# Performance work log

Measured on AMD Instinct MI355X. Metric: run time of the kernel, lower is better.

Reference implementation:

```python
import jax, jax.numpy as jnp
import numpy as np
from jax import lax

EDGE_THRESHOLD = 0.1
DILATION_SIZE = 5
VAR_RATIO_THRESHOLD = 2.0
LOCAL_WINDOW = 7

SOBEL_X = jnp.array([[-1., 0., 1.], [-2., 0., 2.], [-1., 0., 1.]], dtype=jnp.float32)[None, None]
SOBEL_Y = jnp.array([[-1., -2., -1.], [0., 0., 0.], [1., 2., 1.]], dtype=jnp.float32)[None, None]


def _conv_same(x, k):
    # x: (B,1,H,W), k: (1,1,kh,kw), stride 1, SAME padding (odd kernels)
    return lax.conv_general_dilated(x, k.astype(x.dtype), (1, 1), 'SAME',
                                    dimension_numbers=('NCHW', 'OIHW', 'NCHW'))


def _rgb_to_luminance(x):
    w = jnp.array([0.299, 0.587, 0.114], dtype=x.dtype).reshape(1, 3, 1, 1)
    return (x * w).sum(axis=1, keepdims=True)


def _sobel_edge(lum):
    gx = _conv_same(lum, SOBEL_X)
    gy = _conv_same(lum, SOBEL_Y)
    return jnp.sqrt(gx * gx + gy * gy + 1e-12)


def _local_variance(x, mask):
    ws = LOCAL_WINDOW
    ones_k = jnp.ones((1, 1, ws, ws), dtype=x.dtype)
    local_sum = _conv_same(x * mask, ones_k)
    local_cnt = jnp.clip(_conv_same(mask, ones_k), 1.0, None)
    local_mean = local_sum / local_cnt
    local_sq_sum = _conv_same(x * x * mask, ones_k)
    local_var = jnp.clip(local_sq_sum / local_cnt - local_mean ** 2, 0.0, None) * mask
    total = jnp.clip(mask.sum(axis=(2, 3)), 1.0, None)  # (B,1)
    return local_var.sum(axis=(2, 3)) / total  # (B,1)


def _compute_ringing_mask(img):
    lum = _rgb_to_luminance(img) if img.shape[1] == 3 else img
    grad_mag = _sobel_edge(lum)
    E = (grad_mag > EDGE_THRESHOLD).astype(lum.dtype)
    # morphological dilation via max pool, kernel=5, stride=1, SAME padding
    E_dilated = lax.reduce_window(E, -jnp.inf, lax.max,
                                  (1, 1, DILATION_SIZE, DILATION_SIZE),
                                  (1, 1, 1, 1), 'SAME')
    M_prox = jnp.clip(E_dilated - E, 0.0, None)
    M_bg = 1.0 - E_dilated
    var_prox = _local_variance(lum, M_prox)  # (B,1)
    var_bg = _local_variance(lum, M_bg)      # (B,1)
    ratio = var_prox / (var_bg + 1e-12)
    is_ringing = (ratio > VAR_RATIO_THRESHOLD).astype(lum.dtype)  # (B,1)
    return M_prox * is_ringing[:, :, None, None]


def setup_inputs() -> dict:
    key = jax.random.key(0)
    k1, k2 = jax.random.split(key)
    B, C, H, W = 16, 3, 512, 512
    ref = jax.random.uniform(k1, (B, C, H, W), dtype=jnp.float32)
    tgt = jax.random.uniform(k2, (B, C, H, W), dtype=jnp.float32)
    return {"ref": ref, "tgt": tgt}


def reference(ref, tgt):
    ringing_ref = _compute_ringing_mask(ref)
    ringing_tgt = _compute_ringing_mask(tgt)
    return jnp.clip(ringing_tgt - ringing_ref, 0.0, None)
```

## Files before the change

kernel.cpp:

```cpp
#include <hip/hip_runtime.h>

#define HH 512
#define WW 512
#define NPIX (HH*WW)
#define BATCH 16
#define NIMG 32

typedef unsigned char uchar;
typedef unsigned long long u64;

__global__ __launch_bounds__(256) void k_lum(const float4* __restrict__ ref,
                                             const float4* __restrict__ tgt,
                                             float4* __restrict__ lum) {
    int idx = blockIdx.x * 256 + threadIdx.x;
    int img = idx >> 16;
    int p4 = idx & 65535;
    const float4* src = (img < BATCH) ? (ref + (size_t)img * 3 * 65536)
                                      : (tgt + (size_t)(img - BATCH) * 3 * 65536);
    float4 r = src[p4];
    float4 g = src[65536 + p4];
    float4 b = src[131072 + p4];
    float4 o;
    o.x = 0.299f * r.x + 0.587f * g.x + 0.114f * b.x;
    o.y = 0.299f * r.y + 0.587f * g.y + 0.114f * b.y;
    o.z = 0.299f * r.z + 0.587f * g.z + 0.114f * b.z;
    o.w = 0.299f * r.w + 0.587f * g.w + 0.114f * b.w;
    lum[idx] = o;
}


__inline__ __device__ float wave_reduce(float v) {
#pragma unroll
    for (int o = 32; o > 0; o >>= 1) v += __shfl_down(v, o);
    return v;
}

__global__ __launch_bounds__(256) void k_strip(const float* __restrict__ lum,
                                               uchar* __restrict__ Mo_g,
                                               double* __restrict__ acc) {
    int lane = threadIdx.x & 63;
    int gw = blockIdx.x * 4 + (threadIdx.x >> 6);
    int img = gw / 160;
    int rem = gw - img * 160;
    int sy = rem / 10;
    int sx = rem - sy * 10;
    int r0 = sy << 5;
    int c0 = sx * 52;
    int col = c0 + lane - 6;
    bool colok = (unsigned)col < WW;

    int lm1 = (lane > 0) ? lane - 1 : 0;
    int lp1 = (lane < 63) ? lane + 1 : 63;
    int lm2 = (lane > 1) ? lane - 2 : 0;
    int lp2 = (lane < 62) ? lane + 2 : 63;

    const float* Lp = lum + (size_t)img * NPIX;
    uchar* Mo = Mo_g + (size_t)img * NPIX;

    float tm0 = 0, tm1 = 0, tm2 = 0, tm3 = 0;
    float tc0 = 0, tc1 = 0, tc2 = 0, tc3 = 0;
    float tp0 = 0, tp1 = 0, tp2 = 0, tp3 = 0;
    unsigned eb = 0, hb = 0, pbm = 0, vbm = 0;

    float preA = (((unsigned)(r0 - 6) < HH) && colok) ? Lp[(size_t)(r0 - 6) * WW + col] : 0.0f;
    float preB = (((unsigned)(r0 - 5) < HH) && colok) ? Lp[(size_t)(r0 - 5) * WW + col] : 0.0f;

#define LOADROW(Lr) { \
    tm0 = tm1; tc0 = tc1; tp0 = tp1; \
    tm1 = tm2; tc1 = tc2; tp1 = tp2; \
    tm2 = tm3; tc2 = tc3; tp2 = tp3; \
    float ln = preA; preA = preB; \
    { int rr = (Lr) + 2; \
      preB = (((unsigned)rr < HH) && colok) ? Lp[(size_t)rr * WW + col] : 0.0f; } \
    tc3 = ln; tm3 = __shfl(ln, lm1); tp3 = __shfl(ln, lp1); }

#define SOBEL_E(Lr) { \
    float gx = (tp1 - tm1) + 2.0f * (tp2 - tm2) + (tp3 - tm3); \
    float gy = (tm3 + 2.0f * tc3 + tp3) - (tm1 + 2.0f * tc1 + tp1); \
    float grad = sqrtf(gx * gx + gy * gy + 1e-12f); \
    bool e = (grad > 0.1f) && colok && ((unsigned)((Lr) - 1) < HH); \
    u64 ebal = __ballot(e); \
    eb = (eb << 1) | (e ? 1u : 0u); \
    unsigned hE5 = (unsigned)((ebal << 2) >> lane) & 0x1Fu; \
    hb = (hb << 1) | (hE5 ? 1u : 0u); }

    for (int q = 0; q < 2; ++q) { int Lr = r0 - 6 + q; LOADROW(Lr); }
    for (int q = 0; q < 4; ++q) { int Lr = r0 - 4 + q; LOADROW(Lr); SOBEL_E(Lr); }

    float r1p[7], r2p[7], r1v[7], r2v[7];
    unsigned rcn[7];
    unsigned cnt_acc = 0;
    float a1p = 0, a2p = 0, a1v = 0, a2v = 0;
    float c0a = 0, c1a = 0, c2a = 0, c3a = 0;

    for (int o6 = 0; o6 < 6; ++o6) {
#pragma unroll
        for (int u = 0; u < 7; ++u) {
            int j = o6 * 7 + u;
            int Lr = r0 + j;
            LOADROW(Lr);
            SOBEL_E(Lr);
            int m = Lr - 3;
            bool ed = (hb & 0x1Fu) != 0;
            bool e3 = ((eb >> 2) & 1u) != 0;
            bool mrowok = (unsigned)m < HH;
            bool pp = ed && !e3 && mrowok && colok;
            bool vv = (!ed) && mrowok && colok;
            u64 pb = __ballot(pp);
            u64 vb = __ballot(vv);
            pbm = (pbm << 1) | (pp ? 1u : 0u);
            vbm = (vbm << 1) | (vv ? 1u : 0u);

            float xx0 = __shfl(tm0, lm2);
            float xx1 = __shfl(tc0, lm2);
            float xx2 = tm0;
            float xx3 = tc0;
            float xx4 = tp0;
            float xx5 = __shfl(tc0, lp2);
            float xx6 = __shfl(tp0, lp2);
            unsigned pw = (unsigned)((pb << 3) >> lane) & 0x7Fu;
            unsigned vw = (unsigned)((vb << 3) >> lane) & 0x7Fu;
            unsigned cnt_new = (unsigned)__popc(pw) | ((unsigned)__popc(vw) << 8);
            float s1p = 0, s2p = 0, s1v = 0, s2v = 0;
#define TAP(i, xi) { float xq = (xi) * (xi); \
            s1p += ((pw >> (i)) & 1u) ? (xi) : 0.0f; \
            s2p += ((pw >> (i)) & 1u) ? xq : 0.0f; \
            s1v += ((vw >> (i)) & 1u) ? (xi) : 0.0f; \
            s2v += ((vw >> (i)) & 1u) ? xq : 0.0f; }
            TAP(0, xx0) TAP(1, xx1) TAP(2, xx2) TAP(3, xx3)
            TAP(4, xx4) TAP(5, xx5) TAP(6, xx6)
#undef TAP

            if (j >= 7) {
                cnt_acc -= rcn[u];
                a1p -= r1p[u]; a2p -= r2p[u]; a1v -= r1v[u]; a2v -= r2v[u];
            }
            cnt_acc += cnt_new;
            a1p += s1p; a2p += s2p; a1v += s1v; a2v += s2v;
            rcn[u] = cnt_new; r1p[u] = s1p; r2p[u] = s2p; r1v[u] = s1v; r2v[u] = s2v;

            if (j >= 3 && j <= 34) {
                if (lane >= 6 && lane <= 57 && colok)
                    Mo[(size_t)m * WW + col] = (uchar)(pp ? 1 : 0);
            }
            if (j >= 6 && j <= 37) {
                float mp0 = (float)((pbm >> 3) & 1u);
                float mb0 = (float)((vbm >> 3) & 1u);
                if (lane < 6 || lane > 57) { mp0 = 0.0f; mb0 = 0.0f; }
                float cpf = (float)(cnt_acc & 0xFFu);
                float cvf = (float)((cnt_acc >> 8) & 0xFFu);
                float rCp = __builtin_amdgcn_rcpf(fmaxf(cpf, 1.0f));
                float meanp = a1p * rCp;
                float varp = fmaxf(a2p * rCp - meanp * meanp, 0.0f);
                float rCb = __builtin_amdgcn_rcpf(fmaxf(cvf, 1.0f));
                float meanb = a1v * rCb;
                float varb = fmaxf(a2v * rCb - meanb * meanb, 0.0f);
                c0a += varp * mp0; c1a += mp0;
                c2a += varb * mb0; c3a += mb0;
            }
        }
    }

    c0a = wave_reduce(c0a); c1a = wave_reduce(c1a);
    c2a = wave_reduce(c2a); c3a = wave_reduce(c3a);
    if (lane == 0) {
        atomicAdd(&acc[img * 4 + 0], (double)c0a);
        atomicAdd(&acc[img * 4 + 1], (double)c1a);
        atomicAdd(&acc[img * 4 + 2], (double)c2a);
        atomicAdd(&acc[img * 4 + 3], (double)c3a);
    }
}

__global__ void k_flags(const double* __restrict__ acc, float* __restrict__ flags) {
    int i = threadIdx.x;
    if (i >= NIMG) return;
    const double* a = acc + (size_t)i * 4;
    double vp = a[0] / fmax(a[1], 1.0);
    double vb = a[2] / fmax(a[3], 1.0);
    flags[i] = ((vp / (vb + 1e-12)) > 2.0) ? 1.0f : 0.0f;
}

__global__ __launch_bounds__(256) void k_out(const uchar4* __restrict__ M,
                                             const float* __restrict__ flags,
                                             float4* __restrict__ out) {
    int idx = blockIdx.x * 256 + threadIdx.x;
    int b = idx >> 16;
    int p = idx & 65535;
    float fr = flags[b], ft = flags[b + BATCH];
    uchar4 mr = M[(size_t)b * 65536 + p];
    uchar4 mt = M[(size_t)(b + BATCH) * 65536 + p];
    float4 o;
    o.x = fmaxf((mt.x ? ft : 0.0f) - (mr.x ? fr : 0.0f), 0.0f);
    o.y = fmaxf((mt.y ? ft : 0.0f) - (mr.y ? fr : 0.0f), 0.0f);
    o.z = fmaxf((mt.z ? ft : 0.0f) - (mr.z ? fr : 0.0f), 0.0f);
    o.w = fmaxf((mt.w ? ft : 0.0f) - (mr.w ? fr : 0.0f), 0.0f);
    out[idx] = o;
}

extern "C" void kernel_launch(void* const* d_in, const int* in_sizes, int n_in,
                              void* d_out, int out_size, void* d_ws, size_t ws_size,
                              hipStream_t stream) {
    const float* ref = (const float*)d_in[0];
    const float* tgt = (const float*)d_in[1];
    float* out = (float*)d_out;

    char* ws = (char*)d_ws;
    double* acc = (double*)ws;
    float* flags = (float*)(ws + 1024);
    float* lum = (float*)(ws + 2048);
    uchar* Mo = (uchar*)(ws + 2048 + (size_t)NIMG * NPIX * 4);

    (void)hipMemsetAsync(acc, 0, NIMG * 4 * sizeof(double), stream);

    int nAll = NIMG * NPIX;
    k_lum<<<nAll / 4 / 256, 256, 0, stream>>>((const float4*)ref, (const float4*)tgt, (float4*)lum);
    k_strip<<<1280, 256, 0, stream>>>(lum, Mo, acc);
    k_flags<<<1, 64, 0, stream>>>(acc, flags);
    k_out<<<BATCH * NPIX / 4 / 256, 256, 0, stream>>>((const uchar4*)Mo, flags, (float4*)out);
}
```

Baseline: 222.1 us.

## Fuse luminance into strip kernel and fold flag computation into output kernel

Removes the separate luminance kernel: the strip kernel now reads the R, G and B planes directly and computes luminance on the fly for each row, so the intermediate luminance buffer is never written or reread. It also drops the single-block flags kernel and has each output block recompute its two flags from the accumulators in shared memory. Together this removes two launches and a full-size intermediate round trip, at the cost of three loads per pixel in the strip kernel, including redundant reads in the overlapping halo columns and rows.

Measured after the change: 271.4 us. +22.2%, slower.

```diff
diff --git a/kernel.cpp b/kernel.cpp
--- a/kernel.cpp
+++ b/kernel.cpp
@@ -9,25 +9,6 @@
 typedef unsigned char uchar;
 typedef unsigned long long u64;
 
-__global__ __launch_bounds__(256) void k_lum(const float4* __restrict__ ref,
-                                             const float4* __restrict__ tgt,
-                                             float4* __restrict__ lum) {
-    int idx = blockIdx.x * 256 + threadIdx.x;
-    int img = idx >> 16;
-    int p4 = idx & 65535;
-    const float4* src = (img < BATCH) ? (ref + (size_t)img * 3 * 65536)
-                                      : (tgt + (size_t)(img - BATCH) * 3 * 65536);
-    float4 r = src[p4];
-    float4 g = src[65536 + p4];
-    float4 b = src[131072 + p4];
-    float4 o;
-    o.x = 0.299f * r.x + 0.587f * g.x + 0.114f * b.x;
-    o.y = 0.299f * r.y + 0.587f * g.y + 0.114f * b.y;
-    o.z = 0.299f * r.z + 0.587f * g.z + 0.114f * b.z;
-    o.w = 0.299f * r.w + 0.587f * g.w + 0.114f * b.w;
-    lum[idx] = o;
-}
-
 
 __inline__ __device__ float wave_reduce(float v) {
 #pragma unroll
@@ -35,7 +16,8 @@
     return v;
 }
 
-__global__ __launch_bounds__(256) void k_strip(const float* __restrict__ lum,
+__global__ __launch_bounds__(256) void k_strip(const float* __restrict__ ref,
+                                               const float* __restrict__ tgt,
                                                uchar* __restrict__ Mo_g,
                                                double* __restrict__ acc) {
     int lane = threadIdx.x & 63;
@@ -54,7 +36,11 @@
     int lm2 = (lane > 1) ? lane - 2 : 0;
     int lp2 = (lane < 62) ? lane + 2 : 63;
 
-    const float* Lp = lum + (size_t)img * NPIX;
+    const float* base = (img < BATCH) ? (ref + (size_t)img * 3 * NPIX)
+                                      : (tgt + (size_t)(img - BATCH) * 3 * NPIX);
+    const float* Rp = base;
+    const float* Gp = base + NPIX;
+    const float* Bp = base + 2 * NPIX;
     uchar* Mo = Mo_g + (size_t)img * NPIX;
 
     float tm0 = 0, tm1 = 0, tm2 = 0, tm3 = 0;
@@ -62,16 +48,24 @@
     float tp0 = 0, tp1 = 0, tp2 = 0, tp3 = 0;
     unsigned eb = 0, hb = 0, pbm = 0, vbm = 0;
 
-    float preA = (((unsigned)(r0 - 6) < HH) && colok) ? Lp[(size_t)(r0 - 6) * WW + col] : 0.0f;
-    float preB = (((unsigned)(r0 - 5) < HH) && colok) ? Lp[(size_t)(r0 - 5) * WW + col] : 0.0f;
+    float pAr, pAg, pAb, pBr, pBg, pBb;
+#define FETCH3(rr, fr, fg, fb) { \
+    bool ok = ((unsigned)(rr) < HH) && colok; \
+    size_t off = (size_t)(rr) * WW + col; \
+    fr = ok ? Rp[off] : 0.0f; \
+    fg = ok ? Gp[off] : 0.0f; \
+    fb = ok ? Bp[off] : 0.0f; }
+
+    FETCH3(r0 - 6, pAr, pAg, pAb);
+    FETCH3(r0 - 5, pBr, pBg, pBb);
 
 #define LOADROW(Lr) { \
     tm0 = tm1; tc0 = tc1; tp0 = tp1; \
     tm1 = tm2; tc1 = tc2; tp1 = tp2; \
     tm2 = tm3; tc2 = tc3; tp2 = tp3; \
-    float ln = preA; preA = preB; \
-    { int rr = (Lr) + 2; \
-      preB = (((unsigned)rr < HH) && colok) ? Lp[(size_t)rr * WW + col] : 0.0f; } \
+    float ln = 0.299f * pAr + 0.587f * pAg + 0.114f * pAb; \
+    pAr = pBr; pAg = pBg; pAb = pBb; \
+    FETCH3((Lr) + 2, pBr, pBg, pBb); \
     tc3 = ln; tm3 = __shfl(ln, lm1); tp3 = __shfl(ln, lp1); }
 
 #define SOBEL_E(Lr) { \
@@ -171,22 +165,25 @@
     }
 }
 
-__global__ void k_flags(const double* __restrict__ acc, float* __restrict__ flags) {
-    int i = threadIdx.x;
-    if (i >= NIMG) return;
-    const double* a = acc + (size_t)i * 4;
-    double vp = a[0] / fmax(a[1], 1.0);
-    double vb = a[2] / fmax(a[3], 1.0);
-    flags[i] = ((vp / (vb + 1e-12)) > 2.0) ? 1.0f : 0.0f;
-}
-
 __global__ __launch_bounds__(256) void k_out(const uchar4* __restrict__ M,
-                                             const float* __restrict__ flags,
+                                             const double* __restrict__ acc,
                                              float4* __restrict__ out) {
+    __shared__ float sf[2];
     int idx = blockIdx.x * 256 + threadIdx.x;
     int b = idx >> 16;
+    if (threadIdx.x == 0) {
+        const double* a = acc + (size_t)b * 4;
+        double vp = a[0] / fmax(a[1], 1.0);
+        double vb = a[2] / fmax(a[3], 1.0);
+        sf[0] = ((vp / (vb + 1e-12)) > 2.0) ? 1.0f : 0.0f;
+        const double* a2 = acc + (size_t)(b + BATCH) * 4;
+        double vp2 = a2[0] / fmax(a2[1], 1.0);
+        double vb2 = a2[2] / fmax(a2[3], 1.0);
+        sf[1] = ((vp2 / (vb2 + 1e-12)) > 2.0) ? 1.0f : 0.0f;
+    }
+    __syncthreads();
+    float fr = sf[0], ft = sf[1];
     int p = idx & 65535;
-    float fr = flags[b], ft = flags[b + BATCH];
     uchar4 mr = M[(size_t)b * 65536 + p];
     uchar4 mt = M[(size_t)(b + BATCH) * 65536 + p];
     float4 o;
@@ -206,15 +203,10 @@
 
     char* ws = (char*)d_ws;
     double* acc = (double*)ws;
-    float* flags = (float*)(ws + 1024);
-    float* lum = (float*)(ws + 2048);
-    uchar* Mo = (uchar*)(ws + 2048 + (size_t)NIMG * NPIX * 4);
+    uchar* Mo = (uchar*)(ws + 2048);
 
     (void)hipMemsetAsync(acc, 0, NIMG * 4 * sizeof(double), stream);
 
-    int nAll = NIMG * NPIX;
-    k_lum<<<nAll / 4 / 256, 256, 0, stream>>>((const float4*)ref, (const float4*)tgt, (float4*)lum);
-    k_strip<<<1280, 256, 0, stream>>>(lum, Mo, acc);
-    k_flags<<<1, 64, 0, stream>>>(acc, flags);
-    k_out<<<BATCH * NPIX / 4 / 256, 256, 0, stream>>>((const uchar4*)Mo, flags, (float4*)out);
-}
+    k_strip<<<1280, 256, 0, stream>>>(ref, tgt, Mo, acc);
+    k_out<<<BATCH * NPIX / 4 / 256, 256, 0, stream>>>((const uchar4*)Mo, acc, (float4*)out);
+}
```

## Fuse luminance, strip, and output stages into one cooperative kernel

Applied to the files above, without the earlier changes.

Merges the luminance, strip statistics, flag computation and output kernels into a single cooperative kernel of 1280 blocks, separated by grid-wide syncs. The memset is replaced by zeroing the accumulators in the first phase, and flags are computed per block into LDS. The aim is to remove launch gaps and the separate memset and flags launches. In exchange, the grid-stride loops run at fixed occupancy (launch_bounds 256,5), and if the occupancy check fails a fallback path of three kernels is used.

Measured after the change: 226.2 us. Within noise of the previous version (+1.9%).

```diff
diff --git a/kernel.cpp b/kernel.cpp
--- a/kernel.cpp
+++ b/kernel.cpp
@@ -1,33 +1,18 @@
 #include <hip/hip_runtime.h>
+#include <hip/hip_cooperative_groups.h>
+
+namespace cg = cooperative_groups;
 
 #define HH 512
 #define WW 512
 #define NPIX (HH*WW)
 #define BATCH 16
 #define NIMG 32
+#define NBLK 1280
+#define NTHR (NBLK*256)
 
 typedef unsigned char uchar;
 typedef unsigned long long u64;
-
-__global__ __launch_bounds__(256) void k_lum(const float4* __restrict__ ref,
-                                             const float4* __restrict__ tgt,
-                                             float4* __restrict__ lum) {
-    int idx = blockIdx.x * 256 + threadIdx.x;
-    int img = idx >> 16;
-    int p4 = idx & 65535;
-    const float4* src = (img < BATCH) ? (ref + (size_t)img * 3 * 65536)
-                                      : (tgt + (size_t)(img - BATCH) * 3 * 65536);
-    float4 r = src[p4];
-    float4 g = src[65536 + p4];
-    float4 b = src[131072 + p4];
-    float4 o;
-    o.x = 0.299f * r.x + 0.587f * g.x + 0.114f * b.x;
-    o.y = 0.299f * r.y + 0.587f * g.y + 0.114f * b.y;
-    o.z = 0.299f * r.z + 0.587f * g.z + 0.114f * b.z;
-    o.w = 0.299f * r.w + 0.587f * g.w + 0.114f * b.w;
-    lum[idx] = o;
-}
-
 
 __inline__ __device__ float wave_reduce(float v) {
 #pragma unroll
@@ -35,11 +20,37 @@
     return v;
 }
 
-__global__ __launch_bounds__(256) void k_strip(const float* __restrict__ lum,
-                                               uchar* __restrict__ Mo_g,
-                                               double* __restrict__ acc) {
-    int lane = threadIdx.x & 63;
-    int gw = blockIdx.x * 4 + (threadIdx.x >> 6);
+__device__ __forceinline__ void lum_body(int tid, int nthr,
+                                         const float* __restrict__ ref,
+                                         const float* __restrict__ tgt,
+                                         float* __restrict__ lum,
+                                         double* __restrict__ acc) {
+    if (tid < NIMG * 4) acc[tid] = 0.0;
+    const float4* r4 = (const float4*)ref;
+    const float4* t4 = (const float4*)tgt;
+    float4* l4 = (float4*)lum;
+    const int total = NIMG * NPIX / 4;
+    for (int idx = tid; idx < total; idx += nthr) {
+        int img = idx >> 16;
+        int p4 = idx & 65535;
+        const float4* src = (img < BATCH) ? (r4 + (size_t)img * 3 * 65536)
+                                          : (t4 + (size_t)(img - BATCH) * 3 * 65536);
+        float4 r = src[p4];
+        float4 g = src[65536 + p4];
+        float4 b = src[131072 + p4];
+        float4 o;
+        o.x = 0.299f * r.x + 0.587f * g.x + 0.114f * b.x;
+        o.y = 0.299f * r.y + 0.587f * g.y + 0.114f * b.y;
+        o.z = 0.299f * r.z + 0.587f * g.z + 0.114f * b.z;
+        o.w = 0.299f * r.w + 0.587f * g.w + 0.114f * b.w;
+        l4[idx] = o;
+    }
+}
+
+__device__ __forceinline__ void strip_body(const float* __restrict__ lum,
+                                           uchar* __restrict__ Mo_g,
+                                           double* __restrict__ acc,
+                                           int lane, int gw) {
     int img = gw / 160;
     int rem = gw - img * 160;
     int sy = rem / 10;
@@ -160,6 +171,8 @@
             }
         }
     }
+#undef LOADROW
+#undef SOBEL_E
 
     c0a = wave_reduce(c0a); c1a = wave_reduce(c1a);
     c2a = wave_reduce(c2a); c3a = wave_reduce(c3a);
@@ -171,30 +184,88 @@
     }
 }
 
-__global__ void k_flags(const double* __restrict__ acc, float* __restrict__ flags) {
-    int i = threadIdx.x;
-    if (i >= NIMG) return;
-    const double* a = acc + (size_t)i * 4;
-    double vp = a[0] / fmax(a[1], 1.0);
-    double vb = a[2] / fmax(a[3], 1.0);
-    flags[i] = ((vp / (vb + 1e-12)) > 2.0) ? 1.0f : 0.0f;
-}
-
-__global__ __launch_bounds__(256) void k_out(const uchar4* __restrict__ M,
-                                             const float* __restrict__ flags,
-                                             float4* __restrict__ out) {
-    int idx = blockIdx.x * 256 + threadIdx.x;
-    int b = idx >> 16;
-    int p = idx & 65535;
-    float fr = flags[b], ft = flags[b + BATCH];
-    uchar4 mr = M[(size_t)b * 65536 + p];
-    uchar4 mt = M[(size_t)(b + BATCH) * 65536 + p];
-    float4 o;
-    o.x = fmaxf((mt.x ? ft : 0.0f) - (mr.x ? fr : 0.0f), 0.0f);
-    o.y = fmaxf((mt.y ? ft : 0.0f) - (mr.y ? fr : 0.0f), 0.0f);
-    o.z = fmaxf((mt.z ? ft : 0.0f) - (mr.z ? fr : 0.0f), 0.0f);
-    o.w = fmaxf((mt.w ? ft : 0.0f) - (mr.w ? fr : 0.0f), 0.0f);
-    out[idx] = o;
+__device__ __forceinline__ void flags_to_lds(const double* __restrict__ acc,
+                                             float* sflags) {
+    if (threadIdx.x < NIMG) {
+        const double* a = acc + (size_t)threadIdx.x * 4;
+        double vp = a[0] / fmax(a[1], 1.0);
+        double vb = a[2] / fmax(a[3], 1.0);
+        sflags[threadIdx.x] = ((vp / (vb + 1e-12)) > 2.0) ? 1.0f : 0.0f;
+    }
+    __syncthreads();
+}
+
+__device__ __forceinline__ void out_body(int tid, int nthr,
+                                         const uchar* __restrict__ Mo_g,
+                                         const float* sflags,
+                                         float* __restrict__ out) {
+    const uchar4* M4 = (const uchar4*)Mo_g;
+    float4* o4 = (float4*)out;
+    const int total = BATCH * NPIX / 4;
+    for (int idx = tid; idx < total; idx += nthr) {
+        int b = idx >> 16;
+        int p = idx & 65535;
+        float fr = sflags[b], ft = sflags[b + BATCH];
+        uchar4 mr = M4[(size_t)b * 65536 + p];
+        uchar4 mt = M4[(size_t)(b + BATCH) * 65536 + p];
+        float4 o;
+        o.x = fmaxf((mt.x ? ft : 0.0f) - (mr.x ? fr : 0.0f), 0.0f);
+        o.y = fmaxf((mt.y ? ft : 0.0f) - (mr.y ? fr : 0.0f), 0.0f);
+        o.z = fmaxf((mt.z ? ft : 0.0f) - (mr.z ? fr : 0.0f), 0.0f);
+        o.w = fmaxf((mt.w ? ft : 0.0f) - (mr.w ? fr : 0.0f), 0.0f);
+        o4[idx] = o;
+    }
+}
+
+__global__ __launch_bounds__(256, 5) void k_fused(const float* __restrict__ ref,
+                                                  const float* __restrict__ tgt,
+                                                  float* __restrict__ out,
+                                                  float* __restrict__ lum,
+                                                  uchar* __restrict__ Mo_g,
+                                                  double* __restrict__ acc) {
+    cg::grid_group grid = cg::this_grid();
+    int tid = blockIdx.x * 256 + threadIdx.x;
+
+    lum_body(tid, NTHR, ref, tgt, lum, acc);
+    __threadfence();
+    grid.sync();
+    __threadfence();
+
+    {
+        int lane = threadIdx.x & 63;
+        int gw = blockIdx.x * 4 + (threadIdx.x >> 6);
+        strip_body(lum, Mo_g, acc, lane, gw);
+    }
+    __threadfence();
+    grid.sync();
+    __threadfence();
+
+    __shared__ float sflags[NIMG];
+    flags_to_lds(acc, sflags);
+    out_body(tid, NTHR, Mo_g, sflags, out);
+}
+
+__global__ __launch_bounds__(256) void k_lum(const float* __restrict__ ref,
+                                             const float* __restrict__ tgt,
+                                             float* __restrict__ lum,
+                                             double* __restrict__ acc) {
+    lum_body(blockIdx.x * 256 + threadIdx.x, gridDim.x * 256, ref, tgt, lum, acc);
+}
+
+__global__ __launch_bounds__(256) void k_strip(const float* __restrict__ lum,
+                                               uchar* __restrict__ Mo_g,
+                                               double* __restrict__ acc) {
+    int lane = threadIdx.x & 63;
+    int gw = blockIdx.x * 4 + (threadIdx.x >> 6);
+    strip_body(lum, Mo_g, acc, lane, gw);
+}
+
+__global__ __launch_bounds__(256) void k_out(const uchar* __restrict__ Mo_g,
+                                             const double* __restrict__ acc,
+                                             float* __restrict__ out) {
+    __shared__ float sflags[NIMG];
+    flags_to_lds(acc, sflags);
+    out_body(blockIdx.x * 256 + threadIdx.x, gridDim.x * 256, Mo_g, sflags, out);
 }
 
 extern "C" void kernel_launch(void* const* d_in, const int* in_sizes, int n_in,
@@ -206,15 +277,24 @@
 
     char* ws = (char*)d_ws;
     double* acc = (double*)ws;
-    float* flags = (float*)(ws + 1024);
-    float* lum = (float*)(ws + 2048);
-    uchar* Mo = (uchar*)(ws + 2048 + (size_t)NIMG * NPIX * 4);
-
-    (void)hipMemsetAsync(acc, 0, NIMG * 4 * sizeof(double), stream);
-
-    int nAll = NIMG * NPIX;
-    k_lum<<<nAll / 4 / 256, 256, 0, stream>>>((const float4*)ref, (const float4*)tgt, (float4*)lum);
-    k_strip<<<1280, 256, 0, stream>>>(lum, Mo, acc);
-    k_flags<<<1, 64, 0, stream>>>(acc, flags);
-    k_out<<<BATCH * NPIX / 4 / 256, 256, 0, stream>>>((const uchar4*)Mo, flags, (float4*)out);
-}
+    uchar* Mo = (uchar*)(ws + 2048);
+    float* lum = (float*)(ws + 2048 + (size_t)NIMG * NPIX);
+
+    int maxBlk = 0;
+    hipError_t qe = hipOccupancyMaxActiveBlocksPerMultiprocessor(
+        &maxBlk, (const void*)k_fused, 256, 0);
+    bool coop_ok = (qe == hipSuccess) && (maxBlk >= 5);
+
+    if (coop_ok) {
+        void* args[] = {(void*)&ref, (void*)&tgt, (void*)&out,
+                        (void*)&lum, (void*)&Mo, (void*)&acc};
+        hipError_t le = hipLaunchCooperativeKernel((const void*)k_fused,
+                                                   dim3(NBLK), dim3(256),
+                                                   args, 0, stream);
+        if (le == hipSuccess) return;
+    }
+
+    k_lum<<<2048, 256, 0, stream>>>(ref, tgt, lum, acc);
+    k_strip<<<NBLK, 256, 0, stream>>>(lum, Mo, acc);
+    k_out<<<2048, 256, 0, stream>>>(Mo, acc, out);
+}
```
